# Kernel tuning notes

Measured on AMD Instinct MI355X. Metric: run time of the kernel, lower is better.

Reference implementation:

```python
import jax, jax.numpy as jnp
import numpy as np

N_NODES = 100000
N_EDGES = 1600000
IN_F = 128
OUT_F = 32
HEADS = 2
NEG_SLOPE = 0.2  # DGL GATConv default leaky_relu negative slope


def setup_inputs() -> dict:
    key = jax.random.key(0)
    ks = jax.random.split(key, 12)
    x = jax.random.normal(ks[0], (N_NODES, IN_F), dtype=jnp.float32)
    src = jax.random.randint(ks[1], (N_EDGES,), 0, N_NODES, dtype=jnp.int32)
    dst = jax.random.randint(ks[2], (N_EDGES,), 0, N_NODES, dtype=jnp.int32)
    # GATConv params: fc weight [IN_F, HEADS*OUT_F], attn_l/attn_r [HEADS, OUT_F], bias [HEADS*OUT_F]
    s = 1.0 / np.sqrt(IN_F)
    W = jax.random.normal(ks[3], (IN_F, HEADS * OUT_F), dtype=jnp.float32) * s
    attn_l = jax.random.normal(ks[4], (HEADS, OUT_F), dtype=jnp.float32) * s
    attn_r = jax.random.normal(ks[5], (HEADS, OUT_F), dtype=jnp.float32) * s
    bias_gat = jnp.zeros((HEADS * OUT_F,), dtype=jnp.float32)
    # MLPPredictor: lin1 (2*OUT_F -> OUT_F), lin2 (OUT_F -> 1)
    s1 = 1.0 / np.sqrt(2 * OUT_F)
    W1 = jax.random.normal(ks[6], (2 * OUT_F, OUT_F), dtype=jnp.float32) * s1
    b1 = jnp.zeros((OUT_F,), dtype=jnp.float32)
    s2 = 1.0 / np.sqrt(OUT_F)
    W2 = jax.random.normal(ks[7], (OUT_F, 1), dtype=jnp.float32) * s2
    b2 = jnp.zeros((1,), dtype=jnp.float32)
    return {"x": x, "W": W, "attn_l": attn_l, "attn_r": attn_r,
            "bias_gat": bias_gat, "W1": W1, "b1": b1, "W2": W2, "b2": b2,
            "src": src, "dst": dst}


def _forward(x, W, attn_l, attn_r, bias_gat, W1, b1, W2, b2, src, dst):
    # --- GATConv(in, out, 2 heads) ---
    feat = (x @ W).reshape(N_NODES, HEADS, OUT_F)           # [N,H,F]
    el = jnp.einsum('nhf,hf->nh', feat, attn_l)             # [N,H]
    er = jnp.einsum('nhf,hf->nh', feat, attn_r)             # [N,H]
    e = jax.nn.leaky_relu(el[src] + er[dst], NEG_SLOPE)     # [E,H]
    # edge softmax over incoming edges of each dst node (numerically stable)
    m = jax.ops.segment_max(e, dst, num_segments=N_NODES)   # [N,H]
    ex = jnp.exp(e - m[dst])                                # [E,H]
    denom = jax.ops.segment_sum(ex, dst, num_segments=N_NODES)  # [N,H]
    alpha = ex / denom[dst]                                 # [E,H]
    msg = feat[src] * alpha[:, :, None]                     # [E,H,F]
    rst = jax.ops.segment_sum(msg, dst, num_segments=N_NODES)   # [N,H,F]
    rst = rst + bias_gat.reshape(HEADS, OUT_F)
    h = jax.nn.relu(jnp.mean(rst, axis=1))                  # [N,F]
    # --- MLPPredictor: per-edge concat(src,dst) -> lin1 -> lin2 (no activation) ---
    hcat = jnp.concatenate([h[src], h[dst]], axis=1)        # [E,2F]
    score = (hcat @ W1 + b1) @ W2 + b2                      # [E,1]
    return score


def reference(x, W, attn_l, attn_r, bias_gat, W1, b1, W2, b2, src, dst):
    return _forward(x, W, attn_l, attn_r, bias_gat, W1, b1, W2, b2, src, dst)
```

## Files before the change

kernel.cpp:

```cpp
#include <hip/hip_runtime.h>
#include <hip/hip_fp16.h>

#define N_NODES 100000
#define N_EDGES 1600000
#define IN_F 128
#define OUT_F 32
#define HEADS 2
#define HO 64

#define NBUCK 782
#define BIN_BLOCKS 200
#define BIN_THREADS 1024
#define EPB (N_EDGES / BIN_BLOCKS)
#define CAP 36
#define LCAP 2368

typedef __attribute__((ext_vector_type(8))) _Float16 half8;
typedef __attribute__((ext_vector_type(4))) _Float16 half4v;
typedef __attribute__((ext_vector_type(4))) float    f32x4;

#define XPAD 136

__global__ void wprep_k(const float* __restrict__ W,
                        const float* __restrict__ W1, const float* __restrict__ b1,
                        const float* __restrict__ W2, const float* __restrict__ b2,
                        _Float16* __restrict__ Wt16, float* __restrict__ wcomb,
                        float* __restrict__ ccomb){
  int tid = threadIdx.x;
  if (tid < HO){
    float a = 0.f;
    for (int k = 0; k < OUT_F; ++k) a = fmaf(W1[tid*OUT_F + k], W2[k], a);
    wcomb[tid] = a;
  }
  if (tid == HO){
    float a = 0.f;
    for (int k = 0; k < OUT_F; ++k) a = fmaf(b1[k], W2[k], a);
    *ccomb = a + b2[0];
  }
  for (int i = tid; i < 2048; i += 256){
    int k  = i >> 4;
    int c4 = (i & 15) * 4;
    float4 v = ((const float4*)W)[i];
    Wt16[(c4+0)*IN_F + k] = (_Float16)v.x;
    Wt16[(c4+1)*IN_F + k] = (_Float16)v.y;
    Wt16[(c4+2)*IN_F + k] = (_Float16)v.z;
    Wt16[(c4+3)*IN_F + k] = (_Float16)v.w;
  }
}

__global__ __launch_bounds__(256) void feat_k(
                       const float* __restrict__ x, const _Float16* __restrict__ Wt16,
                       const float* __restrict__ attn_l, const float* __restrict__ attn_r,
                       __half* __restrict__ feat16, float* __restrict__ el, float* __restrict__ er){
  __shared__ __align__(16) _Float16 Ws[64*XPAD];
  __shared__ __align__(16) _Float16 xs[64*XPAD];
  int tid = threadIdx.x;
  int node0 = blockIdx.x*64;

  for (int i = tid; i < 2048; i += 256){
    int c = i >> 5, k4 = i & 31;
    *(uint2*)&Ws[c*XPAD + k4*4] = ((const uint2*)Wt16)[i];
  }
  for (int i = tid; i < 2048; i += 256){
    int ln = i >> 5, kq = i & 31;
    int n = node0 + ln;
    float4 v = (n < N_NODES) ? ((const float4*)x)[(size_t)n*32 + kq]
                             : make_float4(0.f,0.f,0.f,0.f);
    half4v hv = { (_Float16)v.x, (_Float16)v.y, (_Float16)v.z, (_Float16)v.w };
    *(half4v*)&xs[ln*XPAD + kq*4] = hv;
  }
  __syncthreads();

  int w = tid >> 6, lane = tid & 63;
  int row_base = w*16;
  int lr = lane & 15, lg = lane >> 4;
  f32x4 acc0 = {0.f,0.f,0.f,0.f}, acc1 = {0.f,0.f,0.f,0.f};
  f32x4 acc2 = {0.f,0.f,0.f,0.f}, acc3 = {0.f,0.f,0.f,0.f};

  #pragma unroll
  for (int kk = 0; kk < 4; ++kk){
    int ko = kk*32 + lg*8;
    half8 a  = *(const half8*)&xs[(row_base + lr)*XPAD + ko];
    half8 b0 = *(const half8*)&Ws[( 0 + lr)*XPAD + ko];
    half8 b1 = *(const half8*)&Ws[(16 + lr)*XPAD + ko];
    half8 b2 = *(const half8*)&Ws[(32 + lr)*XPAD + ko];
    half8 b3 = *(const half8*)&Ws[(48 + lr)*XPAD + ko];
    acc0 = __builtin_amdgcn_mfma_f32_16x16x32_f16(a, b0, acc0, 0, 0, 0);
    acc1 = __builtin_amdgcn_mfma_f32_16x16x32_f16(a, b1, acc1, 0, 0, 0);
    acc2 = __builtin_amdgcn_mfma_f32_16x16x32_f16(a, b2, acc2, 0, 0, 0);
    acc3 = __builtin_amdgcn_mfma_f32_16x16x32_f16(a, b3, acc3, 0, 0, 0);
  }

  float al0 = attn_l[ 0 + lr], al1 = attn_l[16 + lr];
  float al2 = attn_l[32 + lr], al3 = attn_l[48 + lr];
  float ar0 = attn_r[ 0 + lr], ar1 = attn_r[16 + lr];
  float ar2 = attn_r[32 + lr], ar3 = attn_r[48 + lr];

  #pragma unroll
  for (int r = 0; r < 4; ++r){
    int n = node0 + row_base + lg*4 + r;
    float f0 = acc0[r], f1 = acc1[r], f2 = acc2[r], f3 = acc3[r];
    float p0 = f0*al0 + f1*al1, p1 = f2*al2 + f3*al3;
    float q0 = f0*ar0 + f1*ar1, q1 = f2*ar2 + f3*ar3;
    #pragma unroll
    for (int off = 1; off < 16; off <<= 1){
      p0 += __shfl_xor(p0, off); p1 += __shfl_xor(p1, off);
      q0 += __shfl_xor(q0, off); q1 += __shfl_xor(q1, off);
    }
    if (n < N_NODES){
      size_t base = (size_t)n*HO;
      feat16[base +  0 + lr] = __float2half_rn(f0);
      feat16[base + 16 + lr] = __float2half_rn(f1);
      feat16[base + 32 + lr] = __float2half_rn(f2);
      feat16[base + 48 + lr] = __float2half_rn(f3);
      if (lr == 0){
        *(float2*)&el[n*HEADS] = make_float2(p0, p1);
        *(float2*)&er[n*HEADS] = make_float2(q0, q1);
      }
    }
  }
}

__global__ void bin_k(const int* __restrict__ src, const int* __restrict__ dst,
                      const float* __restrict__ el, const float* __restrict__ er,
                      int* __restrict__ counts, uint2* __restrict__ stg){
  __shared__ int cnt[NBUCK];
  int tid = threadIdx.x, blk = blockIdx.x;
  for (int i = tid; i < NBUCK; i += BIN_THREADS) cnt[i] = 0;
  __syncthreads();
  const int4* s4p = (const int4*)(src + blk*EPB);
  const int4* d4p = (const int4*)(dst + blk*EPB);
  for (int i = tid; i < EPB/4; i += BIN_THREADS){
    int4 s4 = s4p[i];
    int4 d4 = d4p[i];
    int ss[4] = {s4.x, s4.y, s4.z, s4.w};
    int dd[4] = {d4.x, d4.y, d4.z, d4.w};
    #pragma unroll
    for (int u = 0; u < 4; ++u){
      int s = ss[u], d = dd[u];
      float2 elv = *(const float2*)&el[s*HEADS];
      float2 erv = *(const float2*)&er[d*HEADS];
      float t0 = elv.x + erv.x, t1 = elv.y + erv.y;
      t0 = t0 > 0.f ? t0 : 0.2f*t0;
      t1 = t1 > 0.f ? t1 : 0.2f*t1;
      __half2 ex2 = __float22half2_rn(make_float2(__expf(t0), __expf(t1)));
      int b = d >> 7;
      int slot = atomicAdd(&cnt[b], 1);
      if (slot < CAP)
        stg[((size_t)blk*NBUCK + b)*CAP + slot] =
          make_uint2(((unsigned int)s << 7) | (unsigned int)(d & 127),
                     *(const unsigned int*)&ex2);
    }
  }
  __syncthreads();
  for (int i = tid; i < NBUCK; i += BIN_THREADS)
    counts[blk*NBUCK + i] = cnt[i] < CAP ? cnt[i] : CAP;
}

__global__ void __launch_bounds__(512, 8) scatter_agg_k(
                              const int* __restrict__ counts, const uint2* __restrict__ stg,
                              const __half* __restrict__ feat16, const float* __restrict__ bias,
                              const float* __restrict__ wcomb,
                              float* __restrict__ s1, float* __restrict__ s2){
  __shared__ uint2 lsev[LCAP];
  __shared__ int hist[128];
  __shared__ int start[128];
  __shared__ int cur[128];
  __shared__ int wtot[2];
  int b = blockIdx.x;
  int tid = threadIdx.x;
  int w = tid >> 6, lane = tid & 63;
  if (tid < 128) hist[tid] = 0;
  __syncthreads();

  int grp = tid >> 3, gl = tid & 7;
  for (int blk = grp; blk < BIN_BLOCKS; blk += 64){
    int n = counts[blk*NBUCK + b];
    const unsigned int* segx = (const unsigned int*)(stg + ((size_t)blk*NBUCK + b)*CAP);
    for (int j = gl; j < n; j += 8){
      unsigned int rx = segx[2*j];
      atomicAdd(&hist[rx & 127], 1);
    }
  }
  __syncthreads();

  int v = 0, inc = 0;
  if (tid < 128){
    v = hist[tid];
    inc = v;
    #pragma unroll
    for (int off = 1; off < 64; off <<= 1){
      int t = __shfl_up(inc, off);
      if (lane >= off) inc += t;
    }
    if (lane == 63) wtot[w] = inc;
  }
  __syncthreads();
  if (tid == 0){ int t0 = wtot[0]; wtot[0] = 0; wtot[1] = t0; }
  __syncthreads();
  if (tid < 128){
    int excl = wtot[w] + inc - v;
    start[tid] = excl;
    cur[tid] = excl;
  }
  __syncthreads();

  for (int blk = grp; blk < BIN_BLOCKS; blk += 64){
    int n = counts[blk*NBUCK + b];
    const uint2* seg = stg + ((size_t)blk*NBUCK + b)*CAP;
    for (int j = gl; j < n; j += 8){
      uint2 r = seg[j];
      int pos = atomicAdd(&cur[r.x & 127], 1);
      if (pos < LCAP) lsev[pos] = make_uint2(r.x >> 7, r.y);
    }
  }
  __syncthreads();

  int g  = lane >> 4;
  int c4 = lane & 15;
  int h  = (c4 >= 8);
  float b0v = bias[c4*4 + 0], b1v = bias[c4*4 + 1], b2v = bias[c4*4 + 2], b3v = bias[c4*4 + 3];
  int f0 = (c4 & 7)*4;
  int wo = (h ? 32 : 0) + f0;
  float m0 = wcomb[wo], m1 = wcomb[wo+1], m2 = wcomb[wo+2], m3 = wcomb[wo+3];
  for (int i = 0; i < 16; ++i){
    int nl = w*16 + i;
    int node = (b << 7) + nl;
    if (node >= N_NODES) break;
    int s0 = start[nl];
    int e0 = cur[nl]; if (e0 > LCAP) e0 = LCAP;
    int deg = e0 - s0; if (deg < 0) deg = 0;

    float a0=0.f, a1=0.f, a2=0.f, a3=0.f, dn=0.f;
    for (int j0 = 0; j0 < deg; j0 += 16){
      int jA = j0 + g, jB = j0 + 4 + g, jC = j0 + 8 + g, jD = j0 + 12 + g;
      float alA=0.f, alB=0.f, alC=0.f, alD=0.f;
      int snA=0, snB=0, snC=0, snD=0;
      if (jA < deg){ uint2 r = lsev[s0+jA]; snA = r.x;
        float2 e = __half22float2(*(const __half2*)&r.y); alA = (h?e.y:e.x); }
      if (jB < deg){ uint2 r = lsev[s0+jB]; snB = r.x;
        float2 e = __half22float2(*(const __half2*)&r.y); alB = (h?e.y:e.x); }
      if (jC < deg){ uint2 r = lsev[s0+jC]; snC = r.x;
        float2 e = __half22float2(*(const __half2*)&r.y); alC = (h?e.y:e.x); }
      if (jD < deg){ uint2 r = lsev[s0+jD]; snD = r.x;
        float2 e = __half22float2(*(const __half2*)&r.y); alD = (h?e.y:e.x); }
      dn += alA + alB + alC + alD;
      uint2 vA = *(const uint2*)(feat16 + (size_t)snA*HO + c4*4);
      uint2 vB = *(const uint2*)(feat16 + (size_t)snB*HO + c4*4);
      uint2 vC = *(const uint2*)(feat16 + (size_t)snC*HO + c4*4);
      uint2 vD = *(const uint2*)(feat16 + (size_t)snD*HO + c4*4);
      float2 fA01 = __half22float2(*(const __half2*)&vA.x);
      float2 fA23 = __half22float2(*(const __half2*)&vA.y);
      float2 fB01 = __half22float2(*(const __half2*)&vB.x);
      float2 fB23 = __half22float2(*(const __half2*)&vB.y);
      float2 fC01 = __half22float2(*(const __half2*)&vC.x);
      float2 fC23 = __half22float2(*(const __half2*)&vC.y);
      float2 fD01 = __half22float2(*(const __half2*)&vD.x);
      float2 fD23 = __half22float2(*(const __half2*)&vD.y);
      a0 = fmaf(alA, fA01.x, a0); a0 = fmaf(alB, fB01.x, a0);
      a0 = fmaf(alC, fC01.x, a0); a0 = fmaf(alD, fD01.x, a0);
      a1 = fmaf(alA, fA01.y, a1); a1 = fmaf(alB, fB01.y, a1);
      a1 = fmaf(alC, fC01.y, a1); a1 = fmaf(alD, fD01.y, a1);
      a2 = fmaf(alA, fA23.x, a2); a2 = fmaf(alB, fB23.x, a2);
      a2 = fmaf(alC, fC23.x, a2); a2 = fmaf(alD, fD23.x, a2);
      a3 = fmaf(alA, fA23.y, a3); a3 = fmaf(alB, fB23.y, a3);
      a3 = fmaf(alC, fC23.y, a3); a3 = fmaf(alD, fD23.y, a3);
    }
    a0 += __shfl_xor(a0, 16); a1 += __shfl_xor(a1, 16);
    a2 += __shfl_xor(a2, 16); a3 += __shfl_xor(a3, 16);
    dn += __shfl_xor(dn, 16);
    a0 += __shfl_xor(a0, 32); a1 += __shfl_xor(a1, 32);
    a2 += __shfl_xor(a2, 32); a3 += __shfl_xor(a3, 32);
    dn += __shfl_xor(dn, 32);
    float rh = dn > 0.f ? 1.f/dn : 0.f;
    a0 = fmaf(a0, rh, b0v); a1 = fmaf(a1, rh, b1v);
    a2 = fmaf(a2, rh, b2v); a3 = fmaf(a3, rh, b3v);
    float h0 = 0.5f*(a0 + __shfl_xor(a0, 8)); h0 = fmaxf(h0, 0.f);
    float h1 = 0.5f*(a1 + __shfl_xor(a1, 8)); h1 = fmaxf(h1, 0.f);
    float h2 = 0.5f*(a2 + __shfl_xor(a2, 8)); h2 = fmaxf(h2, 0.f);
    float h3 = 0.5f*(a3 + __shfl_xor(a3, 8)); h3 = fmaxf(h3, 0.f);
    float r = h0*m0 + h1*m1 + h2*m2 + h3*m3;
    r += __shfl_xor(r, 4); r += __shfl_xor(r, 2); r += __shfl_xor(r, 1);
    if (lane == 0)      s1[node] = r;
    else if (lane == 8) s2[node] = r;
  }
}

__global__ void edge_score_k(const int* __restrict__ src, const int* __restrict__ dst,
                             const float* __restrict__ s1, const float* __restrict__ s2,
                             const float* __restrict__ ccomb, float* __restrict__ out){
  int i = blockIdx.x*blockDim.x + threadIdx.x;
  if (i >= N_EDGES/4) return;
  int4 s4 = ((const int4*)src)[i];
  int4 d4 = ((const int4*)dst)[i];
  float c = ccomb[0];
  float4 o;
  o.x = s1[s4.x] + s2[d4.x] + c;
  o.y = s1[s4.y] + s2[d4.y] + c;
  o.z = s1[s4.z] + s2[d4.z] + c;
  o.w = s1[s4.w] + s2[d4.w] + c;
  ((float4*)out)[i] = o;
}

extern "C" void kernel_launch(void* const* d_in, const int* in_sizes, int n_in,
                              void* d_out, int out_size, void* d_ws, size_t ws_size,
                              hipStream_t stream){
  const float* x      = (const float*)d_in[0];
  const float* W      = (const float*)d_in[1];
  const float* attn_l = (const float*)d_in[2];
  const float* attn_r = (const float*)d_in[3];
  const float* bias   = (const float*)d_in[4];
  const float* W1     = (const float*)d_in[5];
  const float* b1     = (const float*)d_in[6];
  const float* W2     = (const float*)d_in[7];
  const float* b2     = (const float*)d_in[8];
  const int*   src    = (const int*)d_in[9];
  const int*   dst    = (const int*)d_in[10];
  float* out = (float*)d_out;

  float* ws = (float*)d_ws;
  size_t off = 0;
  __half* feat16 = (__half*)(ws + off); off += (size_t)N_NODES*HO/2;
  float*  el     = ws + off; off += (size_t)N_NODES*HEADS;
  float*  er     = ws + off; off += (size_t)N_NODES*HEADS;
  float*  s1     = ws + off; off += N_NODES;
  float*  s2     = ws + off; off += N_NODES;
  float*  wcomb  = ws + off; off += 64;
  float*  ccomb  = ws + off; off += 64;
  _Float16* Wt16 = (_Float16*)(ws + off); off += (size_t)HO*IN_F/2;
  int*    counts = (int*)(ws + off); off += (size_t)BIN_BLOCKS*NBUCK;
  off = (off + 1) & ~(size_t)1;
  uint2*  stg    = (uint2*)(ws + off); off += (size_t)2*BIN_BLOCKS*NBUCK*CAP;

  wprep_k<<<1, 256, 0, stream>>>(W, W1, b1, W2, b2, Wt16, wcomb, ccomb);
  feat_k<<<(N_NODES + 63)/64, 256, 0, stream>>>(x, Wt16, attn_l, attn_r, feat16, el, er);
  bin_k<<<BIN_BLOCKS, BIN_THREADS, 0, stream>>>(src, dst, el, er, counts, stg);
  scatter_agg_k<<<NBUCK, 512, 0, stream>>>(counts, stg, feat16, bias, wcomb, s1, s2);
  edge_score_k<<<(N_EDGES/4 + 255)/256, 256, 0, stream>>>(src, dst, s1, s2, ccomb, out);
}
```

Measured before the change: 238.1 us.

## Split aggregation buckets into halves and reduce binning blocks with transposed counts

Binning now uses 64 blocks with a doubled per-bucket capacity, and the count table is stored transposed so each aggregation block loads its counts contiguously into shared memory. The aggregation kernel launches two blocks per 128-node bucket, each handling 64 destination nodes. Each block filters staged edges by half and runs a single-wave scan, which removes the cross-wave prefix step and halves per-block shared memory. In exchange, both halves read the whole staging segment, and fewer binning blocks mean less parallelism and more shared-atomic contention in bin_k.

Result: slower. 262.5 us (+10.3%).

```diff
diff --git a/kernel.cpp b/kernel.cpp
--- a/kernel.cpp
+++ b/kernel.cpp
@@ -9,11 +9,11 @@
 #define HO 64
 
 #define NBUCK 782
-#define BIN_BLOCKS 200
+#define BIN_BLOCKS 64
 #define BIN_THREADS 1024
 #define EPB (N_EDGES / BIN_BLOCKS)
-#define CAP 36
-#define LCAP 2368
+#define CAP 72
+#define LCAPH 1216
 
 typedef __attribute__((ext_vector_type(8))) _Float16 half8;
 typedef __attribute__((ext_vector_type(4))) _Float16 half4v;
@@ -123,7 +123,7 @@
 
 __global__ void bin_k(const int* __restrict__ src, const int* __restrict__ dst,
                       const float* __restrict__ el, const float* __restrict__ er,
-                      int* __restrict__ counts, uint2* __restrict__ stg){
+                      int* __restrict__ counts_t, uint2* __restrict__ stg){
   __shared__ int cnt[NBUCK];
   int tid = threadIdx.x, blk = blockIdx.x;
   for (int i = tid; i < NBUCK; i += BIN_THREADS) cnt[i] = 0;
@@ -154,64 +154,60 @@
   }
   __syncthreads();
   for (int i = tid; i < NBUCK; i += BIN_THREADS)
-    counts[blk*NBUCK + i] = cnt[i] < CAP ? cnt[i] : CAP;
+    counts_t[i*BIN_BLOCKS + blk] = cnt[i] < CAP ? cnt[i] : CAP;
 }
 
 __global__ void __launch_bounds__(512, 8) scatter_agg_k(
-                              const int* __restrict__ counts, const uint2* __restrict__ stg,
+                              const int* __restrict__ counts_t, const uint2* __restrict__ stg,
                               const __half* __restrict__ feat16, const float* __restrict__ bias,
                               const float* __restrict__ wcomb,
                               float* __restrict__ s1, float* __restrict__ s2){
-  __shared__ uint2 lsev[LCAP];
-  __shared__ int hist[128];
-  __shared__ int start[128];
-  __shared__ int cur[128];
-  __shared__ int wtot[2];
-  int b = blockIdx.x;
+  __shared__ uint2 lsev[LCAPH];
+  __shared__ int cnts[BIN_BLOCKS];
+  __shared__ int hist[64];
+  __shared__ int start[64];
+  __shared__ int cur[64];
+  int bh = blockIdx.x;
+  int b = bh >> 1, half = bh & 1;
   int tid = threadIdx.x;
   int w = tid >> 6, lane = tid & 63;
-  if (tid < 128) hist[tid] = 0;
+  if (tid < 64) hist[tid] = 0;
+  if (tid < BIN_BLOCKS) cnts[tid] = counts_t[b*BIN_BLOCKS + tid];
   __syncthreads();
 
   int grp = tid >> 3, gl = tid & 7;
-  for (int blk = grp; blk < BIN_BLOCKS; blk += 64){
-    int n = counts[blk*NBUCK + b];
-    const unsigned int* segx = (const unsigned int*)(stg + ((size_t)blk*NBUCK + b)*CAP);
-    for (int j = gl; j < n; j += 8){
+  int n_seg = cnts[grp];
+  const uint2* seg = stg + ((size_t)grp*NBUCK + b)*CAP;
+
+  {
+    const unsigned int* segx = (const unsigned int*)seg;
+    for (int j = gl; j < n_seg; j += 8){
       unsigned int rx = segx[2*j];
-      atomicAdd(&hist[rx & 127], 1);
-    }
-  }
-  __syncthreads();
-
-  int v = 0, inc = 0;
-  if (tid < 128){
-    v = hist[tid];
-    inc = v;
+      int dl = rx & 127;
+      if ((dl >> 6) == half) atomicAdd(&hist[dl & 63], 1);
+    }
+  }
+  __syncthreads();
+
+  if (tid < 64){
+    int v = hist[tid];
+    int inc = v;
     #pragma unroll
     for (int off = 1; off < 64; off <<= 1){
       int t = __shfl_up(inc, off);
       if (lane >= off) inc += t;
     }
-    if (lane == 63) wtot[w] = inc;
-  }
-  __syncthreads();
-  if (tid == 0){ int t0 = wtot[0]; wtot[0] = 0; wtot[1] = t0; }
-  __syncthreads();
-  if (tid < 128){
-    int excl = wtot[w] + inc - v;
-    start[tid] = excl;
-    cur[tid] = excl;
-  }
-  __syncthreads();
-
-  for (int blk = grp; blk < BIN_BLOCKS; blk += 64){
-    int n = counts[blk*NBUCK + b];
-    const uint2* seg = stg + ((size_t)blk*NBUCK + b)*CAP;
-    for (int j = gl; j < n; j += 8){
-      uint2 r = seg[j];
-      int pos = atomicAdd(&cur[r.x & 127], 1);
-      if (pos < LCAP) lsev[pos] = make_uint2(r.x >> 7, r.y);
+    start[tid] = inc - v;
+    cur[tid] = inc - v;
+  }
+  __syncthreads();
+
+  for (int j = gl; j < n_seg; j += 8){
+    uint2 r = seg[j];
+    int dl = r.x & 127;
+    if ((dl >> 6) == half){
+      int pos = atomicAdd(&cur[dl & 63], 1);
+      if (pos < LCAPH) lsev[pos] = make_uint2(r.x >> 7, r.y);
     }
   }
   __syncthreads();
@@ -223,12 +219,12 @@
   int f0 = (c4 & 7)*4;
   int wo = (h ? 32 : 0) + f0;
   float m0 = wcomb[wo], m1 = wcomb[wo+1], m2 = wcomb[wo+2], m3 = wcomb[wo+3];
-  for (int i = 0; i < 16; ++i){
-    int nl = w*16 + i;
-    int node = (b << 7) + nl;
+  for (int i = 0; i < 8; ++i){
+    int nl = w*8 + i;
+    int node = bh*64 + nl;
     if (node >= N_NODES) break;
     int s0 = start[nl];
-    int e0 = cur[nl]; if (e0 > LCAP) e0 = LCAP;
+    int e0 = cur[nl]; if (e0 > LCAPH) e0 = LCAPH;
     int deg = e0 - s0; if (deg < 0) deg = 0;
 
     float a0=0.f, a1=0.f, a2=0.f, a3=0.f, dn=0.f;
@@ -328,13 +324,13 @@
   float*  wcomb  = ws + off; off += 64;
   float*  ccomb  = ws + off; off += 64;
   _Float16* Wt16 = (_Float16*)(ws + off); off += (size_t)HO*IN_F/2;
-  int*    counts = (int*)(ws + off); off += (size_t)BIN_BLOCKS*NBUCK;
+  int*    counts_t = (int*)(ws + off); off += (size_t)NBUCK*BIN_BLOCKS;
   off = (off + 1) & ~(size_t)1;
   uint2*  stg    = (uint2*)(ws + off); off += (size_t)2*BIN_BLOCKS*NBUCK*CAP;
 
   wprep_k<<<1, 256, 0, stream>>>(W, W1, b1, W2, b2, Wt16, wcomb, ccomb);
   feat_k<<<(N_NODES + 63)/64, 256, 0, stream>>>(x, Wt16, attn_l, attn_r, feat16, el, er);
-  bin_k<<<BIN_BLOCKS, BIN_THREADS, 0, stream>>>(src, dst, el, er, counts, stg);
-  scatter_agg_k<<<NBUCK, 512, 0, stream>>>(counts, stg, feat16, bias, wcomb, s1, s2);
+  bin_k<<<BIN_BLOCKS, BIN_THREADS, 0, stream>>>(src, dst, el, er, counts_t, stg);
+  scatter_agg_k<<<2*NBUCK, 512, 0, stream>>>(counts_t, stg, feat16, bias, wcomb, s1, s2);
   edge_score_k<<<(N_EDGES/4 + 255)/256, 256, 0, stream>>>(src, dst, s1, s2, ccomb, out);
 }
```
